# Performance work log

Measured on AMD Instinct MI355X. Metric: run time of the kernel, lower is better.

Reference implementation:

```python
import jax, jax.numpy as jnp
import numpy as np

N_EDGES = 65536
D = 512          # n_hidden
H = 8            # num_heads
DH = D // H      # head_dim
LN_EPS = 1e-5


def _layernorm(x, g, b):
    m = jnp.mean(x, axis=-1, keepdims=True)
    v = jnp.mean(jnp.square(x - m), axis=-1, keepdims=True)
    return (x - m) * jax.lax.rsqrt(v + LN_EPS) * g + b


def setup_inputs() -> dict:
    key = jax.random.key(0)
    ks = jax.random.split(key, 10)
    s = 1.0 / np.sqrt(D)      # ~kaiming-uniform scale for nn.Linear
    s4 = 1.0 / np.sqrt(4 * D)
    return {
        "query_input": jax.random.normal(ks[0], (N_EDGES, D), jnp.float32),
        "source_input": jax.random.normal(ks[1], (N_EDGES, D), jnp.float32),
        "Wq": jax.random.normal(ks[2], (D, D), jnp.float32) * s,
        "bq": jnp.zeros((D,), jnp.float32),
        "Wk": jax.random.normal(ks[3], (D, D), jnp.float32) * s,
        "bk": jnp.zeros((D,), jnp.float32),
        "Wv": jax.random.normal(ks[4], (D, D), jnp.float32) * s,
        "bv": jnp.zeros((D,), jnp.float32),
        "Wh": jax.random.normal(ks[5], (D, D), jnp.float32) * s,
        "bh": jnp.zeros((D,), jnp.float32),
        "ln_kv_g": jnp.ones((D,), jnp.float32),
        "ln_kv_b": jnp.zeros((D,), jnp.float32),
        "ln_q_g": jnp.ones((D,), jnp.float32),
        "ln_q_b": jnp.zeros((D,), jnp.float32),
        "ln2_g": jnp.ones((D,), jnp.float32),
        "ln2_b": jnp.zeros((D,), jnp.float32),
        "W1": jax.random.normal(ks[6], (D, 4 * D), jnp.float32) * s,
        "b1": jnp.zeros((4 * D,), jnp.float32),
        "W2": jax.random.normal(ks[7], (4 * D, D), jnp.float32) * s4,
        "b2": jnp.zeros((D,), jnp.float32),
    }


def reference(query_input, source_input, Wq, bq, Wk, bk, Wv, bv, Wh, bh,
              ln_kv_g, ln_kv_b, ln_q_g, ln_q_b, ln2_g, ln2_b,
              W1, b1, W2, b2):
    n = query_input.shape[0]
    ln_src = _layernorm(source_input, ln_kv_g, ln_kv_b)
    ln_qry = _layernorm(query_input, ln_q_g, ln_q_b)

    qs = (ln_qry @ Wq + bq).reshape(n, H, DH)
    ks = (ln_src @ Wk + bk).reshape(n, H, DH)
    vs = (ln_src @ Wv + bv).reshape(n, H, DH)

    # torch.norm(qs, p=2) with no dim => GLOBAL Frobenius norm (faithful to source)
    qs = qs / jnp.linalg.norm(qs)
    ks = ks / jnp.linalg.norm(ks)

    nf = jnp.asarray(n, qs.dtype)
    kvs = jnp.einsum('nhd,nhk->hdk', ks, vs)                 # [H, DH, DH]
    # 'nhd,hdd->nhd' : repeated d on kvs takes its DIAGONAL (torch semantics)
    attention_num = jnp.einsum('nhd,hdd->nhd', qs, kvs) + vs * nf
    ks_sum = jnp.sum(ks, axis=0)                             # == einsum('nhd,n->hd', ks, ones)
    normalizer = jnp.einsum('nhd,hd->nh', qs, ks_sum)[..., None] + nf
    attn_output = (attention_num / normalizer).reshape(n, H * DH)

    h_post_attention = attn_output @ Wh + bh
    h_pre_ffn = source_input + h_post_attention              # dropout = identity (eval)
    y = _layernorm(h_pre_ffn, ln2_g, ln2_b)
    h_post_ffn = jax.nn.gelu(y @ W1 + b1, approximate=False) @ W2 + b2
    return h_pre_ffn + h_post_ffn
```

## Files before the change

kernel.cpp:

```cpp
#include <hip/hip_runtime.h>
#include <hip/hip_bf16.h>

#define NROWS 65536
#define LN_EPS 1e-5f

typedef __attribute__((ext_vector_type(8))) short bf16x8;
typedef __attribute__((ext_vector_type(4))) float f32x4;

__device__ __forceinline__ float bf2f(unsigned short u) {
  union { unsigned u; float f; } c; c.u = ((unsigned)u) << 16; return c.f;
}
__device__ __forceinline__ unsigned short f2bf(float f) {
  union { float f; unsigned u; } c; c.f = f;
  return (unsigned short)((c.u + 0x7fffu + ((c.u >> 16) & 1u)) >> 16);
}

__launch_bounds__(256)
__global__ void normcast_k(const float* __restrict__ x, unsigned short* __restrict__ o) {
  int t = threadIdx.x;
  int row = blockIdx.x * 4 + (t >> 6);
  int lane = t & 63;
  const float* p = x + (size_t)row * 512 + lane * 8;
  float4 a = *(const float4*)p;
  float4 b = *(const float4*)(p + 4);
  float s = a.x + a.y + a.z + a.w + b.x + b.y + b.z + b.w;
  float q = a.x*a.x + a.y*a.y + a.z*a.z + a.w*a.w
          + b.x*b.x + b.y*b.y + b.z*b.z + b.w*b.w;
#pragma unroll
  for (int off = 1; off < 64; off <<= 1) {
    s += __shfl_xor(s, off);
    q += __shfl_xor(q, off);
  }
  float mean = s * (1.0f / 512.0f);
  float r = rsqrtf(q * (1.0f / 512.0f) - mean * mean + LN_EPS);
  float va[8] = {a.x, a.y, a.z, a.w, b.x, b.y, b.z, b.w};
  unsigned pk[4];
#pragma unroll
  for (int i = 0; i < 4; ++i) {
    unsigned lo = f2bf((va[2 * i] - mean) * r);
    unsigned hi = f2bf((va[2 * i + 1] - mean) * r);
    pk[i] = lo | (hi << 16);
  }
  uint4 u; u.x = pk[0]; u.y = pk[1]; u.z = pk[2]; u.w = pk[3];
  *(uint4*)(o + (size_t)row * 512 + lane * 8) = u;
}

__launch_bounds__(256)
__global__ void transbf_k(const float* __restrict__ W, const float* __restrict__ g,
                          unsigned short* __restrict__ Wt, int K, int N) {
  __shared__ float tile[32][33];
  int tx = threadIdx.x & 31, ty = threadIdx.x >> 5;
  int n0 = blockIdx.x * 32, k0 = blockIdx.y * 32;
#pragma unroll
  for (int i = 0; i < 4; ++i) {
    int k = k0 + ty + i * 8;
    float gg = g ? g[k] : 1.0f;
    tile[ty + i * 8][tx] = gg * W[(size_t)k * N + n0 + tx];
  }
  __syncthreads();
#pragma unroll
  for (int i = 0; i < 4; ++i) {
    int n = n0 + ty + i * 8;
    Wt[(size_t)n * K + k0 + tx] = f2bf(tile[tx][ty + i * 8]);
  }
}

__launch_bounds__(256)
__global__ void betacalc_k(const float* __restrict__ W, const float* __restrict__ b,
                           const float* __restrict__ bias, float* __restrict__ beta,
                           int K, int N) {
  int n = blockIdx.x * 256 + threadIdx.x;
  float s = 0.f;
  for (int k = 0; k < K; ++k) s += b[k] * W[(size_t)k * N + n];
  beta[n] = s + bias[n];
}

#define M_Q  0
#define M_KV 1
#define M_H  3
#define M_F1 4
#define M_F2 5

template <int MODE>
__launch_bounds__(512, 1)
__global__ void mm8_k(const unsigned short* __restrict__ A,
                      const unsigned short* __restrict__ Bt,
                      void* __restrict__ Ov,
                      const float* __restrict__ beta,
                      const float* __restrict__ src,
                      float* __restrict__ scal,
                      int N, int K) {
  __shared__ __align__(16) unsigned short LDS[65536];
  __shared__ float red[8];
  const int t = threadIdx.x;
  const int lane = t & 63;
  const int wave = t >> 6;
  const int quad = lane >> 4;
  const int l15 = lane & 15;
  const int l7 = lane & 7;
  const int wrow = (wave >> 2) * 128;
  const int wcol = (wave & 3) * 64;

  const unsigned gx = gridDim.x;
  unsigned bid = blockIdx.y * gx + blockIdx.x;
  const unsigned cpx = (gx * gridDim.y) >> 3;
  bid = (bid & 7u) * cpx + (bid >> 3);
  const int m0 = (int)(bid / gx) * 256;
  const int n0 = (int)(bid % gx) * 256;

  const int srow_t = t >> 3;
  const int sslot = t & 7;
  const int sxor = (sslot ^ (srow_t & 7)) * 8;

  f32x4 acc[8][4];
#pragma unroll
  for (int i = 0; i < 8; ++i)
#pragma unroll
    for (int j = 0; j < 4; ++j) acc[i][j] = (f32x4){0.f, 0.f, 0.f, 0.f};

  const int NT = K >> 6;

  for (int tt = 0; tt < NT; ++tt) {
    const int buf = tt & 1;
    const unsigned short* As = LDS + buf * 16384;
    const unsigned short* Bs = LDS + 32768 + buf * 16384;

    if (tt == 0) {
#pragma unroll
      for (int c = 0; c < 4; ++c) {
        const unsigned short* ga = A + (size_t)(m0 + c * 64 + srow_t) * K + sxor;
        __builtin_amdgcn_global_load_lds(
            (const __attribute__((address_space(1))) void*)ga,
            (__attribute__((address_space(3))) void*)(LDS + (c * 64 + wave * 8) * 64), 16, 0, 0);
      }
#pragma unroll
      for (int c = 0; c < 4; ++c) {
        const unsigned short* gb = Bt + (size_t)(n0 + c * 64 + srow_t) * K + sxor;
        __builtin_amdgcn_global_load_lds(
            (const __attribute__((address_space(1))) void*)gb,
            (__attribute__((address_space(3))) void*)(LDS + 32768 + (c * 64 + wave * 8) * 64), 16, 0, 0);
      }
      asm volatile("s_waitcnt vmcnt(0)" ::: "memory");
      __builtin_amdgcn_s_barrier();
    }

    bf16x8 a0[4], a1[4], bfr[4];
#pragma unroll
    for (int x = 0; x < 4; ++x) {
      a0[x]  = *(const bf16x8*)(As + (wrow + x * 16 + l15) * 64 + ((quad ^ l7) * 8));
      bfr[x] = *(const bf16x8*)(Bs + (wcol + x * 16 + l15) * 64 + ((quad ^ l7) * 8));
    }
    if (tt + 1 < NT) {
#pragma unroll
      for (int c = 0; c < 4; ++c) {
        const unsigned short* ga = A + (size_t)(m0 + c * 64 + srow_t) * K + (tt + 1) * 64 + sxor;
        __builtin_amdgcn_global_load_lds(
            (const __attribute__((address_space(1))) void*)ga,
            (__attribute__((address_space(3))) void*)(LDS + (buf ^ 1) * 16384 + (c * 64 + wave * 8) * 64), 16, 0, 0);
      }
    }
    __builtin_amdgcn_s_barrier();
    __builtin_amdgcn_s_setprio(1);
#pragma unroll
    for (int mi = 0; mi < 4; ++mi)
#pragma unroll
      for (int nj = 0; nj < 4; ++nj)
        acc[mi][nj] = __builtin_amdgcn_mfma_f32_16x16x32_bf16(a0[mi], bfr[nj], acc[mi][nj], 0, 0, 0);
    __builtin_amdgcn_s_setprio(0);
    __builtin_amdgcn_s_barrier();

#pragma unroll
    for (int x = 0; x < 4; ++x)
      a1[x] = *(const bf16x8*)(As + (wrow + 64 + x * 16 + l15) * 64 + ((quad ^ l7) * 8));
    if (tt + 1 < NT) {
#pragma unroll
      for (int c = 0; c < 4; ++c) {
        const unsigned short* gb = Bt + (size_t)(n0 + c * 64 + srow_t) * K + (tt + 1) * 64 + sxor;
        __builtin_amdgcn_global_load_lds(
            (const __attribute__((address_space(1))) void*)gb,
            (__attribute__((address_space(3))) void*)(LDS + 32768 + (buf ^ 1) * 16384 + (c * 64 + wave * 8) * 64), 16, 0, 0);
      }
    }
    __builtin_amdgcn_s_barrier();
    __builtin_amdgcn_s_setprio(1);
#pragma unroll
    for (int mi = 0; mi < 4; ++mi)
#pragma unroll
      for (int nj = 0; nj < 4; ++nj)
        acc[4 + mi][nj] = __builtin_amdgcn_mfma_f32_16x16x32_bf16(a1[mi], bfr[nj], acc[4 + mi][nj], 0, 0, 0);
    __builtin_amdgcn_s_setprio(0);
    __builtin_amdgcn_s_barrier();

#pragma unroll
    for (int x = 0; x < 4; ++x) {
      a0[x]  = *(const bf16x8*)(As + (wrow + x * 16 + l15) * 64 + (((4 + quad) ^ l7) * 8));
      bfr[x] = *(const bf16x8*)(Bs + (wcol + x * 16 + l15) * 64 + (((4 + quad) ^ l7) * 8));
    }
    __builtin_amdgcn_s_barrier();
    __builtin_amdgcn_s_setprio(1);
#pragma unroll
    for (int mi = 0; mi < 4; ++mi)
#pragma unroll
      for (int nj = 0; nj < 4; ++nj)
        acc[mi][nj] = __builtin_amdgcn_mfma_f32_16x16x32_bf16(a0[mi], bfr[nj], acc[mi][nj], 0, 0, 0);
    __builtin_amdgcn_s_setprio(0);
    __builtin_amdgcn_s_barrier();

#pragma unroll
    for (int x = 0; x < 4; ++x)
      a1[x] = *(const bf16x8*)(As + (wrow + 64 + x * 16 + l15) * 64 + (((4 + quad) ^ l7) * 8));
    __builtin_amdgcn_s_barrier();
    __builtin_amdgcn_s_setprio(1);
#pragma unroll
    for (int mi = 0; mi < 4; ++mi)
#pragma unroll
      for (int nj = 0; nj < 4; ++nj)
        acc[4 + mi][nj] = __builtin_amdgcn_mfma_f32_16x16x32_bf16(a1[mi], bfr[nj], acc[4 + mi][nj], 0, 0, 0);
    __builtin_amdgcn_s_setprio(0);
    if (tt + 1 < NT) asm volatile("s_waitcnt vmcnt(0)" ::: "memory");
    __builtin_amdgcn_s_barrier();
  }

  float lred = 0.f;
#pragma unroll
  for (int mi = 0; mi < 8; ++mi) {
#pragma unroll
    for (int nj = 0; nj < 4; ++nj) {
      const int col = n0 + wcol + nj * 16 + l15;
      const float bet = beta[col];
      size_t idx = (size_t)(m0 + wrow + mi * 16 + quad * 4) * N + col;
#pragma unroll
      for (int r = 0; r < 4; ++r, idx += N) {
        float v = acc[mi][nj][r] + bet;
        if constexpr (MODE == M_Q) {
          lred += v * v;
          ((unsigned short*)Ov)[idx] = f2bf(v);
        } else if constexpr (MODE == M_H) {
          ((float*)Ov)[idx] = v + src[idx];
        } else if constexpr (MODE == M_F1) {
          float t2 = v * v;
          float y2 = 1.5957691216f * v * __builtin_fmaf(0.044715f, t2, 1.0f);
          float e = __expf(y2);
          float rr = __builtin_amdgcn_rcpf(e + 1.0f);
          ((unsigned short*)Ov)[idx] = f2bf(v - v * rr);
        } else {
          ((float*)Ov)[idx] += v;
        }
      }
    }
  }
  if constexpr (MODE == M_Q) {
#pragma unroll
    for (int off = 32; off > 0; off >>= 1) lred += __shfl_xor(lred, off);
    if (lane == 0) red[wave] = lred;
    __syncthreads();
    if (t == 0) {
      float s = 0.f;
#pragma unroll
      for (int i = 0; i < 8; ++i) s += red[i];
      atomicAdd(scal, s);
    }
  }
}

template <int MODE>
__launch_bounds__(256)
__global__ void mm_k(const unsigned short* __restrict__ A,
                     const unsigned short* __restrict__ Bt,
                     void* __restrict__ Ov,
                     const float* __restrict__ beta,
                     const float* __restrict__ src,
                     float* __restrict__ scal,
                     float* __restrict__ S1,
                     float* __restrict__ S2,
                     int N, int K) {
  __shared__ __align__(16) unsigned short AsBs[2 * 128 * 64];
  __shared__ float red[4];
  unsigned short* As = AsBs;
  unsigned short* Bs = AsBs + 128 * 64;
  const int t = threadIdx.x;
  const int lane = t & 63;
  const int wave = t >> 6;

  const unsigned gx = gridDim.x;
  unsigned bid = blockIdx.y * gx + blockIdx.x;
  const unsigned cpx = (gx * gridDim.y) >> 3;
  bid = (bid & 7u) * cpx + (bid >> 3);
  const int m0 = (int)(bid / gx) * 128;
  const int n0 = (int)(bid % gx) * 128;
  const int g64 = n0 >> 1;

  const int srow = lane >> 3;
  const int sxor = ((lane & 7) ^ srow) * 8;
  const int wm = (wave >> 1) * 64;
  const int wn = (wave & 1) * 64;
  const int quad = lane >> 4;
  const int l15 = lane & 15;
  const int l7 = lane & 7;

  f32x4 acc[4][4];
#pragma unroll
  for (int i = 0; i < 4; ++i)
#pragma unroll
    for (int j = 0; j < 4; ++j) acc[i][j] = (f32x4){0.f, 0.f, 0.f, 0.f};

  for (int k0 = 0; k0 < K; k0 += 64) {
    __syncthreads();
#pragma unroll
    for (int i = 0; i < 4; ++i) {
      int c = wave * 4 + i;
      int grow = c * 8 + srow;
      const unsigned short* ga = A + (size_t)(m0 + grow) * K + k0 + sxor;
      const unsigned short* gb;
      if constexpr (MODE == M_KV) {
        int btrow = (c < 8) ? (g64 + grow) : (512 - 64 + g64 + grow);
        gb = Bt + (size_t)btrow * K + k0 + sxor;
      } else {
        gb = Bt + (size_t)(n0 + grow) * K + k0 + sxor;
      }
      __builtin_amdgcn_global_load_lds(
          (const __attribute__((address_space(1))) void*)ga,
          (__attribute__((address_space(3))) void*)(As + c * 512), 16, 0, 0);
      __builtin_amdgcn_global_load_lds(
          (const __attribute__((address_space(1))) void*)gb,
          (__attribute__((address_space(3))) void*)(Bs + c * 512), 16, 0, 0);
    }
    __syncthreads();
#pragma unroll
    for (int kt = 0; kt < 2; ++kt) {
      const int pb = ((kt * 4 + quad) ^ l7) * 8;
      bf16x8 af[4], bfr[4];
#pragma unroll
      for (int x = 0; x < 4; ++x) {
        af[x]  = *(const bf16x8*)(As + (wm + x * 16 + l15) * 64 + pb);
        bfr[x] = *(const bf16x8*)(Bs + (wn + x * 16 + l15) * 64 + pb);
      }
#pragma unroll
      for (int mi = 0; mi < 4; ++mi)
#pragma unroll
        for (int nj = 0; nj < 4; ++nj)
          acc[mi][nj] = __builtin_amdgcn_mfma_f32_16x16x32_bf16(
              af[mi], bfr[nj], acc[mi][nj], 0, 0, 0);
    }
  }

  float lred = 0.f;
  if constexpr (MODE == M_KV) {
    float* Vx = (float*)AsBs;
    __syncthreads();
    if (wn) {
#pragma unroll
      for (int mi = 0; mi < 4; ++mi) {
#pragma unroll
        for (int nj = 0; nj < 4; ++nj) {
          const int colv = nj * 16 + l15;
          const float bet = beta[512 + g64 + colv];
          size_t idx = (size_t)(m0 + wm + mi * 16 + quad * 4) * 512 + g64 + colv;
#pragma unroll
          for (int r = 0; r < 4; ++r, idx += 512) {
            float v = acc[mi][nj][r] + bet;
            int lr = wm + mi * 16 + quad * 4 + r;
            Vx[lr * 64 + (colv ^ (((lr >> 2) & 3) << 4))] = v;
            ((unsigned short*)Ov)[idx] = f2bf(v);
          }
        }
      }
    }
    __syncthreads();
    if (!wn) {
      float s1[4] = {0.f, 0.f, 0.f, 0.f};
      float s2[4] = {0.f, 0.f, 0.f, 0.f};
#pragma unroll
      for (int mi = 0; mi < 4; ++mi) {
#pragma unroll
        for (int nj = 0; nj < 4; ++nj) {
          const int colv = nj * 16 + l15;
          const float bet = beta[g64 + colv];
#pragma unroll
          for (int r = 0; r < 4; ++r) {
            float v = acc[mi][nj][r] + bet;
            lred += v * v;
            int lr = wm + mi * 16 + quad * 4 + r;
            float vv = Vx[lr * 64 + (colv ^ (((lr >> 2) & 3) << 4))];
            s1[nj] += v * vv;
            s2[nj] += v;
          }
        }
      }
#pragma unroll
      for (int nj = 0; nj < 4; ++nj) {
        s1[nj] += __shfl_xor(s1[nj], 16); s1[nj] += __shfl_xor(s1[nj], 32);
        s2[nj] += __shfl_xor(s2[nj], 16); s2[nj] += __shfl_xor(s2[nj], 32);
      }
      if (quad == 0) {
#pragma unroll
        for (int nj = 0; nj < 4; ++nj) {
          atomicAdd(&S1[g64 + nj * 16 + l15], s1[nj]);
          atomicAdd(&S2[g64 + nj * 16 + l15], s2[nj]);
        }
      }
    }
  }
  if constexpr (MODE == M_KV) {
#pragma unroll
    for (int off = 32; off > 0; off >>= 1) lred += __shfl_xor(lred, off);
    if (lane == 0) red[wave] = lred;
    __syncthreads();
    if (t == 0) atomicAdd(scal, red[0] + red[1] + red[2] + red[3]);
  }
}

__launch_bounds__(256)
__global__ void attn_k(unsigned short* __restrict__ Qb, const unsigned short* __restrict__ Vb,
                       const float* __restrict__ S1, const float* __restrict__ S2,
                       const float* __restrict__ sqq, const float* __restrict__ skk) {
  int t = threadIdx.x;
  int row = blockIdx.x * 4 + (t >> 6);
  int lane = t & 63;
  int c = lane * 8;
  float inv = rsqrtf(sqq[0] * skk[0]);
  const float Nf = (float)NROWS;
  unsigned short* qp = Qb + (size_t)row * 512 + c;
  uint4 qu = *(const uint4*)qp;
  float q[8];
  q[0] = bf2f((unsigned short)(qu.x & 0xffff)); q[1] = bf2f((unsigned short)(qu.x >> 16));
  q[2] = bf2f((unsigned short)(qu.y & 0xffff)); q[3] = bf2f((unsigned short)(qu.y >> 16));
  q[4] = bf2f((unsigned short)(qu.z & 0xffff)); q[5] = bf2f((unsigned short)(qu.z >> 16));
  q[6] = bf2f((unsigned short)(qu.w & 0xffff)); q[7] = bf2f((unsigned short)(qu.w >> 16));
  const unsigned short* vp = Vb + (size_t)row * 512 + c;
  uint4 vu = *(const uint4*)vp;
  float vv[8];
  vv[0] = bf2f((unsigned short)(vu.x & 0xffff)); vv[1] = bf2f((unsigned short)(vu.x >> 16));
  vv[2] = bf2f((unsigned short)(vu.y & 0xffff)); vv[3] = bf2f((unsigned short)(vu.y >> 16));
  vv[4] = bf2f((unsigned short)(vu.z & 0xffff)); vv[5] = bf2f((unsigned short)(vu.z >> 16));
  vv[6] = bf2f((unsigned short)(vu.w & 0xffff)); vv[7] = bf2f((unsigned short)(vu.w >> 16));
  float4 s10 = *(const float4*)(S1 + c), s11 = *(const float4*)(S1 + c + 4);
  float4 s20 = *(const float4*)(S2 + c), s21 = *(const float4*)(S2 + c + 4);
  float s1v[8] = {s10.x, s10.y, s10.z, s10.w, s11.x, s11.y, s11.z, s11.w};
  float s2v[8] = {s20.x, s20.y, s20.z, s20.w, s21.x, s21.y, s21.z, s21.w};
  float part = 0.f;
#pragma unroll
  for (int i = 0; i < 8; ++i) part += q[i] * s2v[i];
  part += __shfl_xor(part, 1);
  part += __shfl_xor(part, 2);
  part += __shfl_xor(part, 4);
  float rn = 1.0f / (inv * part + Nf);
  unsigned pk[4];
#pragma unroll
  for (int i = 0; i < 4; ++i) {
    float o0 = (q[2 * i] * s1v[2 * i] * inv + vv[2 * i] * Nf) * rn;
    float o1 = (q[2 * i + 1] * s1v[2 * i + 1] * inv + vv[2 * i + 1] * Nf) * rn;
    pk[i] = (unsigned)f2bf(o0) | ((unsigned)f2bf(o1) << 16);
  }
  uint4 u; u.x = pk[0]; u.y = pk[1]; u.z = pk[2]; u.w = pk[3];
  *(uint4*)qp = u;
}

extern "C" void kernel_launch(void* const* d_in, const int* in_sizes, int n_in,
                              void* d_out, int out_size, void* d_ws, size_t ws_size,
                              hipStream_t stream) {
  const float* query   = (const float*)d_in[0];
  const float* source  = (const float*)d_in[1];
  const float* Wq      = (const float*)d_in[2];
  const float* bq      = (const float*)d_in[3];
  const float* Wk      = (const float*)d_in[4];
  const float* bk      = (const float*)d_in[5];
  const float* Wv      = (const float*)d_in[6];
  const float* bv      = (const float*)d_in[7];
  const float* Wh      = (const float*)d_in[8];
  const float* bh      = (const float*)d_in[9];
  const float* ln_kv_g = (const float*)d_in[10];
  const float* ln_kv_b = (const float*)d_in[11];
  const float* ln_q_g  = (const float*)d_in[12];
  const float* ln_q_b  = (const float*)d_in[13];
  const float* ln2_g   = (const float*)d_in[14];
  const float* ln2_b   = (const float*)d_in[15];
  const float* W1      = (const float*)d_in[16];
  const float* b1      = (const float*)d_in[17];
  const float* W2      = (const float*)d_in[18];
  const float* b2      = (const float*)d_in[19];
  float* out = (float*)d_out;

  const size_t MB = 1024 * 1024;
  char* w = (char*)d_ws;
  unsigned short* Qn = (unsigned short*)(w + 0 * MB);
  unsigned short* Sn = (unsigned short*)(w + 64 * MB);
  unsigned short* Qb = (unsigned short*)(w + 128 * MB);
  unsigned short* Vb = (unsigned short*)(w + 192 * MB);
  unsigned short* Hn = (unsigned short*)(w + 256 * MB);
  unsigned short* Tb = (unsigned short*)(w + 0 * MB);
  char* wt = w + 384 * MB;
  unsigned short* Wqt = (unsigned short*)wt;
  unsigned short* Wkt = Wqt + 512 * 512;
  unsigned short* Wvt = Wkt + 512 * 512;
  unsigned short* Wht = Wvt + 512 * 512;
  unsigned short* W1t = Wht + 512 * 512;
  unsigned short* W2t = W1t + 512 * 2048;
  float* betaq = (float*)(W2t + 2048 * 512);
  float* betak = betaq + 512;
  float* betav = betak + 512;
  float* betaf = betav + 512;
  float* S1 = betaf + 2048;
  float* S2 = S1 + 512;
  float* SQQ = S2 + 512;
  float* SKK = SQQ + 1;

  hipMemsetAsync(S1, 0, (512 + 512 + 2) * sizeof(float), stream);

  dim3 blk(256);
  dim3 blk8(512);
  normcast_k<<<NROWS / 4, blk, 0, stream>>>(query, Qn);
  normcast_k<<<NROWS / 4, blk, 0, stream>>>(source, Sn);
  transbf_k<<<dim3(16, 16), blk, 0, stream>>>(Wq, ln_q_g, Wqt, 512, 512);
  transbf_k<<<dim3(16, 16), blk, 0, stream>>>(Wk, ln_kv_g, Wkt, 512, 512);
  transbf_k<<<dim3(16, 16), blk, 0, stream>>>(Wv, ln_kv_g, Wvt, 512, 512);
  transbf_k<<<dim3(16, 16), blk, 0, stream>>>(Wh, nullptr, Wht, 512, 512);
  transbf_k<<<dim3(64, 16), blk, 0, stream>>>(W1, ln2_g, W1t, 512, 2048);
  transbf_k<<<dim3(16, 64), blk, 0, stream>>>(W2, nullptr, W2t, 2048, 512);
  betacalc_k<<<2, blk, 0, stream>>>(Wq, ln_q_b, bq, betaq, 512, 512);
  betacalc_k<<<2, blk, 0, stream>>>(Wk, ln_kv_b, bk, betak, 512, 512);
  betacalc_k<<<2, blk, 0, stream>>>(Wv, ln_kv_b, bv, betav, 512, 512);
  betacalc_k<<<8, blk, 0, stream>>>(W1, ln2_b, b1, betaf, 512, 2048);

  mm8_k<M_Q><<<dim3(2, 256), blk8, 0, stream>>>(Qn, Wqt, Qb, betaq, nullptr, SQQ, 512, 512);
  mm_k<M_KV><<<dim3(8, 512), blk, 0, stream>>>(Sn, Wkt, Vb, betak, nullptr, SKK, S1, S2, 512, 512);
  attn_k<<<NROWS / 4, blk, 0, stream>>>(Qb, Vb, S1, S2, SQQ, SKK);
  mm8_k<M_H><<<dim3(2, 256), blk8, 0, stream>>>(Qb, Wht, out, bh, source, nullptr, 512, 512);
  normcast_k<<<NROWS / 4, blk, 0, stream>>>(out, Hn);
  mm8_k<M_F1><<<dim3(8, 256), blk8, 0, stream>>>(Hn, W1t, Tb, betaf, nullptr, nullptr, 2048, 512);
  mm8_k<M_F2><<<dim3(2, 256), blk8, 0, stream>>>(Tb, W2t, out, b2, nullptr, nullptr, 512, 2048);
}
```

Measured before the change: 1.586 ms.

## Restructure GEMM mainloop into 4-stage K=32 LDS ring with one barrier

```diff
diff --git a/kernel.cpp b/kernel.cpp
--- a/kernel.cpp
+++ b/kernel.cpp
@@ -97,7 +97,6 @@
   const int wave = t >> 6;
   const int quad = lane >> 4;
   const int l15 = lane & 15;
-  const int l7 = lane & 7;
   const int wrow = (wave >> 2) * 128;
   const int wcol = (wave & 3) * 64;
 
@@ -108,9 +107,9 @@
   const int m0 = (int)(bid / gx) * 256;
   const int n0 = (int)(bid % gx) * 256;
 
-  const int srow_t = t >> 3;
-  const int sslot = t & 7;
-  const int sxor = (sslot ^ (srow_t & 7)) * 8;
+  const int srow_in = lane >> 2;
+  const int sigma8 = (((lane & 3) ^ ((lane >> 2) & 3) ^ (lane >> 4))) * 8;
+  const int kslot = ((quad ^ ((l15 & 3) ^ ((l15 >> 2) & 3)))) * 8;
 
   f32x4 acc[8][4];
 #pragma unroll
@@ -118,107 +117,59 @@
 #pragma unroll
     for (int j = 0; j < 4; ++j) acc[i][j] = (f32x4){0.f, 0.f, 0.f, 0.f};
 
-  const int NT = K >> 6;
+  const int NT = K >> 5;
+
+  auto stage = [&](int tile) {
+    const int sb = (tile & 3) * 8192;
+    const size_t kof = (size_t)tile * 32 + sigma8;
+#pragma unroll
+    for (int c = 0; c < 2; ++c) {
+      const unsigned short* ga = A + (size_t)(m0 + c * 128 + wave * 16 + srow_in) * K + kof;
+      __builtin_amdgcn_global_load_lds(
+          (const __attribute__((address_space(1))) void*)ga,
+          (__attribute__((address_space(3))) void*)(LDS + sb + (c * 128 + wave * 16) * 32), 16, 0, 0);
+    }
+#pragma unroll
+    for (int c = 0; c < 2; ++c) {
+      const unsigned short* gb = Bt + (size_t)(n0 + c * 128 + wave * 16 + srow_in) * K + kof;
+      __builtin_amdgcn_global_load_lds(
+          (const __attribute__((address_space(1))) void*)gb,
+          (__attribute__((address_space(3))) void*)(LDS + 32768 + sb + (c * 128 + wave * 16) * 32), 16, 0, 0);
+    }
+  };
+
+  stage(0);
+  stage(1);
 
   for (int tt = 0; tt < NT; ++tt) {
-    const int buf = tt & 1;
-    const unsigned short* As = LDS + buf * 16384;
-    const unsigned short* Bs = LDS + 32768 + buf * 16384;
-
-    if (tt == 0) {
-#pragma unroll
-      for (int c = 0; c < 4; ++c) {
-        const unsigned short* ga = A + (size_t)(m0 + c * 64 + srow_t) * K + sxor;
-        __builtin_amdgcn_global_load_lds(
-            (const __attribute__((address_space(1))) void*)ga,
-            (__attribute__((address_space(3))) void*)(LDS + (c * 64 + wave * 8) * 64), 16, 0, 0);
-      }
-#pragma unroll
-      for (int c = 0; c < 4; ++c) {
-        const unsigned short* gb = Bt + (size_t)(n0 + c * 64 + srow_t) * K + sxor;
-        __builtin_amdgcn_global_load_lds(
-            (const __attribute__((address_space(1))) void*)gb,
-            (__attribute__((address_space(3))) void*)(LDS + 32768 + (c * 64 + wave * 8) * 64), 16, 0, 0);
-      }
+    if (tt + 2 < NT) {
+      stage(tt + 2);
+      asm volatile("s_waitcnt vmcnt(8)" ::: "memory");
+    } else if (tt + 1 < NT) {
+      asm volatile("s_waitcnt vmcnt(4)" ::: "memory");
+    } else {
       asm volatile("s_waitcnt vmcnt(0)" ::: "memory");
-      __builtin_amdgcn_s_barrier();
-    }
-
-    bf16x8 a0[4], a1[4], bfr[4];
-#pragma unroll
-    for (int x = 0; x < 4; ++x) {
-      a0[x]  = *(const bf16x8*)(As + (wrow + x * 16 + l15) * 64 + ((quad ^ l7) * 8));
-      bfr[x] = *(const bf16x8*)(Bs + (wcol + x * 16 + l15) * 64 + ((quad ^ l7) * 8));
-    }
-    if (tt + 1 < NT) {
-#pragma unroll
-      for (int c = 0; c < 4; ++c) {
-        const unsigned short* ga = A + (size_t)(m0 + c * 64 + srow_t) * K + (tt + 1) * 64 + sxor;
-        __builtin_amdgcn_global_load_lds(
-            (const __attribute__((address_space(1))) void*)ga,
-            (__attribute__((address_space(3))) void*)(LDS + (buf ^ 1) * 16384 + (c * 64 + wave * 8) * 64), 16, 0, 0);
-      }
-    }
+    }
+    __builtin_amdgcn_sched_barrier(0);
     __builtin_amdgcn_s_barrier();
+
+    const unsigned short* As = LDS + (tt & 3) * 8192;
+    const unsigned short* Bs = LDS + 32768 + (tt & 3) * 8192;
+    bf16x8 a[8], b[4];
+#pragma unroll
+    for (int x = 0; x < 8; ++x)
+      a[x] = *(const bf16x8*)(As + (wrow + x * 16 + l15) * 32 + kslot);
+#pragma unroll
+    for (int x = 0; x < 4; ++x)
+      b[x] = *(const bf16x8*)(Bs + (wcol + x * 16 + l15) * 32 + kslot);
+
     __builtin_amdgcn_s_setprio(1);
 #pragma unroll
-    for (int mi = 0; mi < 4; ++mi)
+    for (int mi = 0; mi < 8; ++mi)
 #pragma unroll
       for (int nj = 0; nj < 4; ++nj)
-        acc[mi][nj] = __builtin_amdgcn_mfma_f32_16x16x32_bf16(a0[mi], bfr[nj], acc[mi][nj], 0, 0, 0);
+        acc[mi][nj] = __builtin_amdgcn_mfma_f32_16x16x32_bf16(a[mi], b[nj], acc[mi][nj], 0, 0, 0);
     __builtin_amdgcn_s_setprio(0);
-    __builtin_amdgcn_s_barrier();
-
-#pragma unroll
-    for (int x = 0; x < 4; ++x)
-      a1[x] = *(const bf16x8*)(As + (wrow + 64 + x * 16 + l15) * 64 + ((quad ^ l7) * 8));
-    if (tt + 1 < NT) {
-#pragma unroll
-      for (int c = 0; c < 4; ++c) {
-        const unsigned short* gb = Bt + (size_t)(n0 + c * 64 + srow_t) * K + (tt + 1) * 64 + sxor;
-        __builtin_amdgcn_global_load_lds(
-            (const __attribute__((address_space(1))) void*)gb,
-            (__attribute__((address_space(3))) void*)(LDS + 32768 + (buf ^ 1) * 16384 + (c * 64 + wave * 8) * 64), 16, 0, 0);
-      }
-    }
-    __builtin_amdgcn_s_barrier();
-    __builtin_amdgcn_s_setprio(1);
-#pragma unroll
-    for (int mi = 0; mi < 4; ++mi)
-#pragma unroll
-      for (int nj = 0; nj < 4; ++nj)
-        acc[4 + mi][nj] = __builtin_amdgcn_mfma_f32_16x16x32_bf16(a1[mi], bfr[nj], acc[4 + mi][nj], 0, 0, 0);
-    __builtin_amdgcn_s_setprio(0);
-    __builtin_amdgcn_s_barrier();
-
-#pragma unroll
-    for (int x = 0; x < 4; ++x) {
-      a0[x]  = *(const bf16x8*)(As + (wrow + x * 16 + l15) * 64 + (((4 + quad) ^ l7) * 8));
-      bfr[x] = *(const bf16x8*)(Bs + (wcol + x * 16 + l15) * 64 + (((4 + quad) ^ l7) * 8));
-    }
-    __builtin_amdgcn_s_barrier();
-    __builtin_amdgcn_s_setprio(1);
-#pragma unroll
-    for (int mi = 0; mi < 4; ++mi)
-#pragma unroll
-      for (int nj = 0; nj < 4; ++nj)
-        acc[mi][nj] = __builtin_amdgcn_mfma_f32_16x16x32_bf16(a0[mi], bfr[nj], acc[mi][nj], 0, 0, 0);
-    __builtin_amdgcn_s_setprio(0);
-    __builtin_amdgcn_s_barrier();
-
-#pragma unroll
-    for (int x = 0; x < 4; ++x)
-      a1[x] = *(const bf16x8*)(As + (wrow + 64 + x * 16 + l15) * 64 + (((4 + quad) ^ l7) * 8));
-    __builtin_amdgcn_s_barrier();
-    __builtin_amdgcn_s_setprio(1);
-#pragma unroll
-    for (int mi = 0; mi < 4; ++mi)
-#pragma unroll
-      for (int nj = 0; nj < 4; ++nj)
-        acc[4 + mi][nj] = __builtin_amdgcn_mfma_f32_16x16x32_bf16(a1[mi], bfr[nj], acc[4 + mi][nj], 0, 0, 0);
-    __builtin_amdgcn_s_setprio(0);
-    if (tt + 1 < NT) asm volatile("s_waitcnt vmcnt(0)" ::: "memory");
-    __builtin_amdgcn_s_barrier();
   }
 
   float lred = 0.f;
```

Result: slower. 1.621 ms (+2.2%).
